# Optimization experiments

Hardware: AMD Instinct MI355X
Metric: run time of the kernel (lower is better)

Reference implementation:

```python
import jax, jax.numpy as jnp
import numpy as np

N_NODES = 50000
N_EDGES = 300000
F_IN = 11
D = 256


def _gcn_conv(h, src, dst, deg_inv_sqrt, W, b, n):
    """PyG GCNConv: out = D^{-1/2} (A + I) D^{-1/2} (h W) + b.
    src/dst already include self-loops; deg_inv_sqrt precomputed."""
    norm = deg_inv_sqrt[src] * deg_inv_sqrt[dst]          # [E+N]
    hw = h @ W                                            # [N, D]
    msg = hw[src] * norm[:, None]                         # [E+N, D]
    out = jax.ops.segment_sum(msg, dst, num_segments=n)   # [N, D]
    return out + b


def setup_inputs() -> dict:
    key = jax.random.key(0)
    ks = jax.random.split(key, 8)
    x = jax.random.normal(ks[0], (N_NODES, F_IN), dtype=jnp.float32)
    edge_index = jax.random.randint(ks[1], (2, N_EDGES), 0, N_NODES, dtype=jnp.int32)
    s = 0.05
    W_embed = jax.random.normal(ks[2], (F_IN, D), dtype=jnp.float32) * s
    b_embed = jnp.zeros((D,), dtype=jnp.float32)
    W1 = jax.random.normal(ks[3], (D, D), dtype=jnp.float32) * s
    b1 = jnp.zeros((D,), dtype=jnp.float32)
    W2 = jax.random.normal(ks[4], (D, D), dtype=jnp.float32) * s
    b2 = jnp.zeros((D,), dtype=jnp.float32)
    return {"x": x, "edge_index": edge_index, "W_embed": W_embed, "b_embed": b_embed,
            "W1": W1, "b1": b1, "W2": W2, "b2": b2}


def reference(x, edge_index, W_embed, b_embed, W1, b1, W2, b2):
    n = x.shape[0]
    # add self-loops (PyG GCNConv default add_self_loops=True)
    loop = jnp.arange(n, dtype=edge_index.dtype)
    src = jnp.concatenate([edge_index[0], loop])
    dst = jnp.concatenate([edge_index[1], loop])
    # symmetric normalization: deg over target index with unit edge weights
    deg = jax.ops.segment_sum(jnp.ones(src.shape, dtype=x.dtype), dst, num_segments=n)
    deg_inv_sqrt = jnp.where(deg > 0, jax.lax.rsqrt(jnp.maximum(deg, 1e-12)), 0.0)

    h = jax.nn.relu(x @ W_embed + b_embed)                # embed + relu
    h = jax.nn.relu(_gcn_conv(h, src, dst, deg_inv_sqrt, W1, b1, n))
    h = _gcn_conv(h, src, dst, deg_inv_sqrt, W2, b2, n)
    return h
```

## Files before the change

### kernel.cpp

```cpp
#include <hip/hip_runtime.h>

#define N_NODES 50000
#define N_EDGES 300000
#define N_TOT   350000
#define D       256
#define MPAD    50048
#define SCAN_B  196
#define BLKM    64
#define LGRID   (MPAD / BLKM)

typedef __attribute__((ext_vector_type(8))) short bf16x8;
typedef __attribute__((ext_vector_type(4))) float f32x4;
typedef __attribute__((ext_vector_type(8))) unsigned short u16x8;
typedef __attribute__((ext_vector_type(4))) unsigned short u16x4;

__device__ __forceinline__ float bf2f(unsigned short b) {
    union { unsigned u; float f; } v; v.u = ((unsigned)b) << 16; return v.f;
}
__device__ __forceinline__ unsigned short f2bf(float f) {
    union { float f; unsigned u; } v; v.f = f;
    unsigned u = v.u;
    unsigned r = (u + 0x7FFFu + ((u >> 16) & 1u)) >> 16;
    return (unsigned short)r;
}
__device__ __forceinline__ void g2lds16(const unsigned short* g, unsigned short* l) {
    __builtin_amdgcn_global_load_lds(
        (const __attribute__((address_space(1))) void*)g,
        (__attribute__((address_space(3))) void*)l, 16, 0, 0);
}

__global__ __launch_bounds__(256) void k1_kernel(
        const float* __restrict__ x, const int* __restrict__ ei,
        const float* __restrict__ We, const float* __restrict__ be,
        const float* __restrict__ W1, const float* __restrict__ W2,
        int* __restrict__ cnt,
        unsigned short* __restrict__ Wt1, unsigned short* __restrict__ Wt2,
        unsigned short* __restrict__ hA) {
    int t = threadIdx.x, b = blockIdx.x;
    int tid = b * 256 + t;

    if (tid < N_TOT) {
        int dst = (tid < N_EDGES) ? ei[N_EDGES + tid] : (tid - N_EDGES);
        atomicAdd(&cnt[dst], 1);
    }
    if (tid < 2 * D * D) {
        int wsel = tid >> 16, rem = tid & 65535;
        int tt = rem >> 8, bb = rem & 255;
        const float* W = wsel ? W2 : W1;
        unsigned short* Wt = wsel ? Wt2 : Wt1;
        Wt[bb * D + tt] = f2bf(W[tt * D + bb]);
    }
    float w[11];
    #pragma unroll
    for (int k = 0; k < 11; ++k) w[k] = We[k * D + t];
    float bb = be[t];
    #pragma unroll
    for (int ni = 0; ni < 8; ++ni) {
        int node = b * 8 + ni;
        float acc = 0.f;
        if (node < N_NODES) {
            acc = bb;
            #pragma unroll
            for (int k = 0; k < 11; ++k) acc += x[node * 11 + k] * w[k];
            acc = fmaxf(acc, 0.f);
        }
        hA[(size_t)node * D + t] = f2bf(acc);
    }
}

__global__ __launch_bounds__(256) void k2_kernel(const int* __restrict__ cnt,
                                                 float* __restrict__ dis,
                                                 int* __restrict__ locs,
                                                 int* __restrict__ bsum,
                                                 int* __restrict__ done) {
    __shared__ int ws[4];
    __shared__ int amLast;
    int t = threadIdx.x;
    int lane = t & 63, wv4 = t >> 6;
    int i = blockIdx.x * 256 + t;
    int v = (i < N_NODES) ? cnt[i] : 0;
    if (i < N_NODES) dis[i] = rsqrtf((float)v);
    int s = v;
    #pragma unroll
    for (int d = 1; d < 64; d <<= 1) {
        int u = __shfl_up(s, d, 64);
        if (lane >= d) s += u;
    }
    if (lane == 63) ws[wv4] = s;
    __syncthreads();
    int off = 0;
    #pragma unroll
    for (int k = 0; k < 4; ++k) if (k < wv4) off += ws[k];
    s += off;
    if (i < N_NODES) locs[i] = s;
    if (t == 255) {
        bsum[blockIdx.x] = s;
        __threadfence();
        amLast = (atomicAdd(done, 1) == SCAN_B - 1);
    }
    __syncthreads();
    if (amLast) {
        __threadfence();
        int vv = 0;
        if (t < SCAN_B)
            vv = __hip_atomic_load(&bsum[t], __ATOMIC_RELAXED, __HIP_MEMORY_SCOPE_AGENT);
        int ss = vv;
        #pragma unroll
        for (int d = 1; d < 64; d <<= 1) {
            int u = __shfl_up(ss, d, 64);
            if (lane >= d) ss += u;
        }
        __syncthreads();
        if (lane == 63) ws[wv4] = ss;
        __syncthreads();
        int off2 = 0;
        #pragma unroll
        for (int k = 0; k < 4; ++k) if (k < wv4) off2 += ws[k];
        ss += off2;
        if (t < SCAN_B) bsum[t] = ss - vv;
    }
}

__global__ __launch_bounds__(256) void k3_kernel(const int* __restrict__ ei,
                          const int* __restrict__ locs,
                          const int* __restrict__ bsum, const float* __restrict__ dis,
                          int* __restrict__ fc, int* __restrict__ rowptr,
                          int2* __restrict__ epk) {
    int tid = blockIdx.x * 256 + threadIdx.x;
    if (tid == 0) rowptr[0] = 0;
    if (tid < N_NODES)
        rowptr[tid + 1] = locs[tid] + bsum[tid >> 8];
    if (tid < N_TOT) {
        int src, dst;
        if (tid < N_EDGES) { src = ei[tid]; dst = ei[N_EDGES + tid]; }
        else               { src = dst = tid - N_EDGES; }
        int base = bsum[dst >> 8] + ((dst & 255) ? locs[dst - 1] : 0);
        int pos = base + atomicAdd(&fc[dst], 1);
        epk[pos] = make_int2(src, __float_as_int(dis[src] * dis[dst]));
    }
}

__global__ __launch_bounds__(256, 3) void layer_kernel(
        const unsigned short* __restrict__ hw,
        const int* __restrict__ rowptr,
        const int2* __restrict__ epk,
        const unsigned short* __restrict__ Bt,
        const float* __restrict__ bias,
        unsigned short* __restrict__ out_bf,
        float* __restrict__ out_f32,
        int mode) {
    __shared__ unsigned short lA[BLKM * D];
    __shared__ unsigned short lB[D * 32];
    int t = threadIdx.x;
    int bid = blockIdx.x;
    int wid = t >> 6, lane = t & 63;
    int h = lane >> 5, hl = lane & 31;
    int hw8 = wid * 2 + h;
    int m0 = bid * BLKM;

    #pragma unroll
    for (int j2 = 0; j2 < 4; ++j2) {
        int idx = j2 * 256 + t;
        int n = idx >> 2, c = idx & 3;
        int cs = c ^ ((n >> 1) & 3);
        g2lds16(Bt + (size_t)n * D + cs * 8, lB + idx * 8);
    }

    for (int j = 0; j < 8; ++j) {
        int nn = hw8 * 8 + j;
        int node = m0 + nn;
        float acc[8] = {};
        if (node < N_NODES) {
            int s0 = rowptr[node], s1 = rowptr[node + 1];
            for (int base = s0; base < s1; base += 8) {
                int idx = base + (hl & 7);
                int srcl = 0; float nml = 0.f;
                if (idx < s1) {
                    int2 ep = epk[idx];
                    srcl = ep.x; nml = __int_as_float(ep.y);
                }
                int se[8]; float ne[8]; u16x8 rw[8];
                #pragma unroll
                for (int e = 0; e < 8; ++e) {
                    se[e] = __shfl(srcl, h * 32 + e, 64);
                    ne[e] = __shfl(nml,  h * 32 + e, 64);
                }
                #pragma unroll
                for (int e = 0; e < 8; ++e)
                    rw[e] = *(const u16x8*)(hw + (size_t)se[e] * D + hl * 8);
                #pragma unroll
                for (int e = 0; e < 8; ++e)
                    #pragma unroll
                    for (int k = 0; k < 8; ++k) acc[k] += ne[e] * bf2f(rw[e][k]);
            }
        }
        u16x8 o;
        #pragma unroll
        for (int k = 0; k < 8; ++k) o[k] = f2bf(acc[k]);
        int chunk = (hl & ~7) | ((hl ^ nn) & 7);
        *(u16x8*)(lA + nn * D + chunk * 8) = o;
    }

    __syncthreads();

    int q = lane >> 4, r = lane & 15;
    int noff = wid * 64;
    f32x4 acc4[4][4] = {};
    for (int st = 0; st < 8; ++st) {
        bf16x8 af[4], bfr[4];
        #pragma unroll
        for (int mt = 0; mt < 4; ++mt) {
            int row = mt * 16 + r;
            int ch = st * 4 + q;
            int chs = (ch & ~7) | ((ch ^ row) & 7);
            af[mt] = *(const bf16x8*)(lA + row * D + chs * 8);
        }
        #pragma unroll
        for (int nt = 0; nt < 4; ++nt) {
            int n = noff + nt * 16 + r;
            int cb = q ^ ((n >> 1) & 3);
            bfr[nt] = *(const bf16x8*)(lB + n * 32 + cb * 8);
        }
        #pragma unroll
        for (int mt = 0; mt < 4; ++mt)
            #pragma unroll
            for (int nt = 0; nt < 4; ++nt)
                acc4[mt][nt] = __builtin_amdgcn_mfma_f32_16x16x32_bf16(
                    bfr[nt], af[mt], acc4[mt][nt], 0, 0, 0);
        if (st < 7) {
            __syncthreads();
            int kk = (st + 1) * 32;
            #pragma unroll
            for (int j2 = 0; j2 < 4; ++j2) {
                int idx = j2 * 256 + t;
                int n = idx >> 2, c = idx & 3;
                int cs = c ^ ((n >> 1) & 3);
                g2lds16(Bt + (size_t)n * D + kk + cs * 8, lB + idx * 8);
            }
            __syncthreads();
        }
    }

    #pragma unroll
    for (int mt = 0; mt < 4; ++mt) {
        int mrow = m0 + mt * 16 + r;
        if (mrow >= N_NODES) continue;
        #pragma unroll
        for (int nt = 0; nt < 4; ++nt) {
            int col = noff + nt * 16 + (q << 2);
            float4 bv = *(const float4*)(bias + col);
            float v[4] = { acc4[mt][nt][0] + bv.x, acc4[mt][nt][1] + bv.y,
                           acc4[mt][nt][2] + bv.z, acc4[mt][nt][3] + bv.w };
            if (mode) {
                u16x4 o;
                #pragma unroll
                for (int i = 0; i < 4; ++i) o[i] = f2bf(fmaxf(v[i], 0.f));
                *(u16x4*)(out_bf + (size_t)mrow * D + col) = o;
            } else {
                float4 o = { v[0], v[1], v[2], v[3] };
                *(float4*)(out_f32 + (size_t)mrow * D + col) = o;
            }
        }
    }
}

extern "C" void kernel_launch(void* const* d_in, const int* in_sizes, int n_in,
                              void* d_out, int out_size, void* d_ws, size_t ws_size,
                              hipStream_t stream) {
    const float* x  = (const float*)d_in[0];
    const int*   ei = (const int*)d_in[1];
    const float* We = (const float*)d_in[2];
    const float* be = (const float*)d_in[3];
    const float* W1 = (const float*)d_in[4];
    const float* b1 = (const float*)d_in[5];
    const float* W2 = (const float*)d_in[6];
    const float* b2 = (const float*)d_in[7];
    float* out = (float*)d_out;

    char* w = (char*)d_ws;
    auto alloc = [&](size_t bytes) {
        char* p = w;
        w += (bytes + 255) & ~(size_t)255;
        return p;
    };
    int*            cnt    = (int*)alloc((size_t)N_NODES * 4);
    int*            fc     = (int*)alloc((size_t)N_NODES * 4);
    int*            done   = (int*)alloc(4);
    size_t zero_span = (size_t)((char*)(done + 64) - (char*)cnt);
    int*            rowptr = (int*)alloc((size_t)(N_NODES + 1) * 4);
    int*            locs   = (int*)alloc((size_t)N_NODES * 4);
    int*            bsum   = (int*)alloc((size_t)SCAN_B * 4);
    float*          dis    = (float*)alloc((size_t)N_NODES * 4);
    int2*           epk    = (int2*)alloc((size_t)N_TOT * 8);
    unsigned short* Wt1    = (unsigned short*)alloc((size_t)D * D * 2);
    unsigned short* Wt2    = (unsigned short*)alloc((size_t)D * D * 2);
    unsigned short* hA     = (unsigned short*)alloc((size_t)MPAD * D * 2);
    unsigned short* h1     = (unsigned short*)alloc((size_t)MPAD * D * 2);

    hipMemsetAsync(cnt, 0, zero_span, stream);
    k1_kernel<<<MPAD / 8, 256, 0, stream>>>(x, ei, We, be, W1, W2, cnt, Wt1, Wt2, hA);
    k2_kernel<<<SCAN_B, 256, 0, stream>>>(cnt, dis, locs, bsum, done);
    k3_kernel<<<(N_TOT + 255) / 256, 256, 0, stream>>>(ei, locs, bsum, dis, fc,
                                                       rowptr, epk);
    layer_kernel<<<LGRID, 256, 0, stream>>>(hA, rowptr, epk, Wt1, b1,
                                            h1, nullptr, 1);
    layer_kernel<<<LGRID, 256, 0, stream>>>(h1, rowptr, epk, Wt2, b2,
                                            nullptr, out, 0);
}
```

Measured before the change: 245.7 us.

## Stage block edge list in LDS and read GEMM weights directly from global

The layer kernel now copies the block's contiguous CSR edge range and row pointers into shared memory up front, so each half-wave reads edges from LDS instead of loading and shuffling them. The weight tile for the MFMA GEMM is read straight from global memory into registers, which drops the per-k-step LDS staging and its two barriers. Occupancy is raised to 4 waves per SIMD. In exchange, blocks whose edge count exceeds the LDS buffer fall back to global edge reads, and the weight fragments now depend on cache hits from global loads.

```diff
diff --git a/kernel.cpp b/kernel.cpp
--- a/kernel.cpp
+++ b/kernel.cpp
@@ -8,6 +8,7 @@
 #define SCAN_B  196
 #define BLKM    64
 #define LGRID   (MPAD / BLKM)
+#define EMAX    896
 
 typedef __attribute__((ext_vector_type(8))) short bf16x8;
 typedef __attribute__((ext_vector_type(4))) float f32x4;
@@ -22,11 +23,6 @@
     unsigned u = v.u;
     unsigned r = (u + 0x7FFFu + ((u >> 16) & 1u)) >> 16;
     return (unsigned short)r;
-}
-__device__ __forceinline__ void g2lds16(const unsigned short* g, unsigned short* l) {
-    __builtin_amdgcn_global_load_lds(
-        (const __attribute__((address_space(1))) void*)g,
-        (__attribute__((address_space(3))) void*)l, 16, 0, 0);
 }
 
 __global__ __launch_bounds__(256) void k1_kernel(
@@ -140,7 +136,7 @@
     }
 }
 
-__global__ __launch_bounds__(256, 3) void layer_kernel(
+__global__ __launch_bounds__(256, 4) void layer_kernel(
         const unsigned short* __restrict__ hw,
         const int* __restrict__ rowptr,
         const int2* __restrict__ epk,
@@ -150,49 +146,51 @@
         float* __restrict__ out_f32,
         int mode) {
     __shared__ unsigned short lA[BLKM * D];
-    __shared__ unsigned short lB[D * 32];
+    __shared__ int2 eL[EMAX];
+    __shared__ int rL[BLKM + 1];
     int t = threadIdx.x;
     int bid = blockIdx.x;
     int wid = t >> 6, lane = t & 63;
     int h = lane >> 5, hl = lane & 31;
     int hw8 = wid * 2 + h;
     int m0 = bid * BLKM;
-
-    #pragma unroll
-    for (int j2 = 0; j2 < 4; ++j2) {
-        int idx = j2 * 256 + t;
-        int n = idx >> 2, c = idx & 3;
-        int cs = c ^ ((n >> 1) & 3);
-        g2lds16(Bt + (size_t)n * D + cs * 8, lB + idx * 8);
-    }
+    int mEnd = m0 + BLKM; if (mEnd > N_NODES) mEnd = N_NODES;
+
+    int s0b = rowptr[m0];
+    int s1b = rowptr[mEnd];
+    int nE = s1b - s0b;
+    bool useL = (nE <= EMAX);
+    if (t <= BLKM) {
+        int idx = m0 + t;
+        rL[t] = rowptr[idx > N_NODES ? N_NODES : idx];
+    }
+    if (useL)
+        for (int i = t; i < nE; i += 256) eL[i] = epk[s0b + i];
+    __syncthreads();
 
     for (int j = 0; j < 8; ++j) {
         int nn = hw8 * 8 + j;
-        int node = m0 + nn;
+        int s0 = rL[nn], s1 = rL[nn + 1];
+        int deg = s1 - s0;
+        int ls0 = s0 - s0b;
         float acc[8] = {};
-        if (node < N_NODES) {
-            int s0 = rowptr[node], s1 = rowptr[node + 1];
-            for (int base = s0; base < s1; base += 8) {
-                int idx = base + (hl & 7);
-                int srcl = 0; float nml = 0.f;
-                if (idx < s1) {
-                    int2 ep = epk[idx];
-                    srcl = ep.x; nml = __int_as_float(ep.y);
-                }
-                int se[8]; float ne[8]; u16x8 rw[8];
+        for (int off = 0; off < deg; off += 8) {
+            int se[8]; float ne[8];
+            #pragma unroll
+            for (int e = 0; e < 8; ++e) {
+                int idx = off + e;
+                int2 ep = make_int2(0, 0);
+                if (idx < deg) ep = useL ? eL[ls0 + idx] : epk[s0 + idx];
+                se[e] = ep.x; ne[e] = __int_as_float(ep.y);
+            }
+            u16x8 rw[8];
+            #pragma unroll
+            for (int e = 0; e < 8; ++e)
+                rw[e] = *(const u16x8*)(hw + (size_t)se[e] * D + hl * 8);
+            #pragma unroll
+            for (int e = 0; e < 8; ++e)
                 #pragma unroll
-                for (int e = 0; e < 8; ++e) {
-                    se[e] = __shfl(srcl, h * 32 + e, 64);
-                    ne[e] = __shfl(nml,  h * 32 + e, 64);
-                }
-                #pragma unroll
-                for (int e = 0; e < 8; ++e)
-                    rw[e] = *(const u16x8*)(hw + (size_t)se[e] * D + hl * 8);
-                #pragma unroll
-                for (int e = 0; e < 8; ++e)
-                    #pragma unroll
-                    for (int k = 0; k < 8; ++k) acc[k] += ne[e] * bf2f(rw[e][k]);
-            }
+                for (int k = 0; k < 8; ++k) acc[k] += ne[e] * bf2f(rw[e][k]);
         }
         u16x8 o;
         #pragma unroll
@@ -205,9 +203,14 @@
 
     int q = lane >> 4, r = lane & 15;
     int noff = wid * 64;
+    const unsigned short* Bw = Bt + (size_t)(noff + r) * D + q * 8;
     f32x4 acc4[4][4] = {};
+    #pragma unroll 1
     for (int st = 0; st < 8; ++st) {
         bf16x8 af[4], bfr[4];
+        #pragma unroll
+        for (int nt = 0; nt < 4; ++nt)
+            bfr[nt] = *(const bf16x8*)(Bw + (size_t)(nt * 16) * D + st * 32);
         #pragma unroll
         for (int mt = 0; mt < 4; ++mt) {
             int row = mt * 16 + r;
@@ -216,29 +219,11 @@
             af[mt] = *(const bf16x8*)(lA + row * D + chs * 8);
         }
         #pragma unroll
-        for (int nt = 0; nt < 4; ++nt) {
-            int n = noff + nt * 16 + r;
-            int cb = q ^ ((n >> 1) & 3);
-            bfr[nt] = *(const bf16x8*)(lB + n * 32 + cb * 8);
-        }
-        #pragma unroll
         for (int mt = 0; mt < 4; ++mt)
             #pragma unroll
             for (int nt = 0; nt < 4; ++nt)
                 acc4[mt][nt] = __builtin_amdgcn_mfma_f32_16x16x32_bf16(
                     bfr[nt], af[mt], acc4[mt][nt], 0, 0, 0);
-        if (st < 7) {
-            __syncthreads();
-            int kk = (st + 1) * 32;
-            #pragma unroll
-            for (int j2 = 0; j2 < 4; ++j2) {
-                int idx = j2 * 256 + t;
-                int n = idx >> 2, c = idx & 3;
-                int cs = c ^ ((n >> 1) & 3);
-                g2lds16(Bt + (size_t)n * D + kk + cs * 8, lB + idx * 8);
-            }
-            __syncthreads();
-        }
     }
 
     #pragma unroll
```

New measurement: 235.4 us. 1.04x faster.
